# Performance work log

Hardware: AMD Instinct MI355X
Metric: run time of the kernel (lower is better)

## Reference

```python
import jax, jax.numpy as jnp
import numpy as np

B, BARS, BEATS, FRAC = 64, 16, 4, 8
IN_F = 10 * 47 * 2  # 940
LIN_OUT = 100
BEAT_H = 16
BAR_H = 32


def _p(key, shape, scale=0.05):
    return jax.random.normal(key, shape, dtype=jnp.float32) * scale


def setup_inputs() -> dict:
    key = jax.random.key(0)
    ks = jax.random.split(key, 16)
    return {
        "channels": jax.random.normal(ks[0], (B, BARS, BEATS, FRAC, 10, 2, 47), dtype=jnp.float32),
        "lin_w": _p(ks[1], (LIN_OUT, IN_F)),
        "lin_b": _p(ks[2], (LIN_OUT,)),
        # beats LSTM (unidirectional), PyTorch gate order i,f,g,o
        "b_wih": _p(ks[3], (4 * BEAT_H, LIN_OUT)),
        "b_whh": _p(ks[4], (4 * BEAT_H, BEAT_H)),
        "b_bih": _p(ks[5], (4 * BEAT_H,)),
        "b_bhh": _p(ks[6], (4 * BEAT_H,)),
        # bars LSTM, bidirectional: forward (f_) and reverse (r_) directions
        "f_wih": _p(ks[7], (4 * BAR_H, BEAT_H)),
        "f_whh": _p(ks[8], (4 * BAR_H, BAR_H)),
        "f_bih": _p(ks[9], (4 * BAR_H,)),
        "f_bhh": _p(ks[10], (4 * BAR_H,)),
        "r_wih": _p(ks[11], (4 * BAR_H, BEAT_H)),
        "r_whh": _p(ks[12], (4 * BAR_H, BAR_H)),
        "r_bih": _p(ks[13], (4 * BAR_H,)),
        "r_bhh": _p(ks[14], (4 * BAR_H,)),
    }


def lstm(x, wih, whh, bih, bhh):
    """PyTorch-semantics LSTM, batch_first. x: [N, T, F] -> h_seq [N, T, H]."""
    N = x.shape[0]
    H = whh.shape[1]
    # precompute input contribution for all timesteps
    xg = jnp.einsum('ntf,gf->ntg', x, wih) + (bih + bhh)  # [N, T, 4H]

    def step(carry, xt):
        h, c = carry
        gates = xt + h @ whh.T  # [N, 4H]
        i, f, g, o = jnp.split(gates, 4, axis=-1)
        c = jax.nn.sigmoid(f) * c + jax.nn.sigmoid(i) * jnp.tanh(g)
        h = jax.nn.sigmoid(o) * jnp.tanh(c)
        return (h, c), h

    h0 = jnp.zeros((N, H), x.dtype)
    _, hs = jax.lax.scan(step, (h0, h0), jnp.swapaxes(xg, 0, 1))  # [T, N, H]
    return jnp.swapaxes(hs, 0, 1)


def bilstm(x, f_wih, f_whh, f_bih, f_bhh, r_wih, r_whh, r_bih, r_bhh):
    fwd = lstm(x, f_wih, f_whh, f_bih, f_bhh)
    bwd = jnp.flip(lstm(jnp.flip(x, axis=1), r_wih, r_whh, r_bih, r_bhh), axis=1)
    return jnp.concatenate([fwd, bwd], axis=-1)


def reference(channels, lin_w, lin_b,
              b_wih, b_whh, b_bih, b_bhh,
              f_wih, f_whh, f_bih, f_bhh,
              r_wih, r_whh, r_bih, r_bhh):
    # channels: [B, bars, beats, frac, 10, 2, 47]
    x = jnp.swapaxes(channels, -1, -2)  # [..., 10, 47, 2]
    x = x.reshape(*x.shape[:4], IN_F)   # squash dims 4..6 -> 940
    x = jax.nn.relu(x @ lin_w.T + lin_b)  # [B, bars, beats, frac, 100]

    # Distributed depth=2: fold (B, bars, beats) into batch, seq over frac
    xb = x.reshape(B * BARS * BEATS, FRAC, LIN_OUT)
    beats = lstm(xb, b_wih, b_whh, b_bih, b_bhh)
    beats = beats.reshape(B, BARS, BEATS, FRAC, BEAT_H)

    # last fraction hidden state, then Distributed depth=1 over beats axis
    xl = beats[:, :, :, -1].reshape(B * BARS, BEATS, BEAT_H)
    bars = bilstm(xl, f_wih, f_whh, f_bih, f_bhh, r_wih, r_whh, r_bih, r_bhh)
    bars = bars.reshape(B, BARS, BEATS, 2 * BAR_H)
    return beats, bars
```

## Files before the change

### kernel.cpp

```cpp
#include <hip/hip_runtime.h>
#include <hip/hip_bf16.h>

typedef float f32x4 __attribute__((ext_vector_type(4)));
typedef short bf16x8 __attribute__((ext_vector_type(8)));

#define MFMA16(a, b, c) __builtin_amdgcn_mfma_f32_16x16x32_bf16(a, b, c, 0, 0, 0)

constexpr int K1  = 940;
constexpr int KP2 = 1024;
constexpr int NP  = 112;
constexpr int OSL = 136;
constexpr int BSR = 72;

__device__ __forceinline__ float sigf(float x) { return 1.f / (1.f + __expf(-x)); }
__device__ __forceinline__ float tanhfast(float x) { return 2.f / (1.f + __expf(-2.f * x)) - 1.f; }

__device__ __forceinline__ short f2b(float x) {
  __hip_bfloat16 b = __float2bfloat16(x);
  return *reinterpret_cast<short*>(&b);
}

__global__ void prep_kernel(const float* __restrict__ lin_w,
                            const float* __restrict__ b_wih,
                            __hip_bfloat16* __restrict__ w2,
                            __hip_bfloat16* __restrict__ bw2) {
  int idx = blockIdx.x * 256 + threadIdx.x;
  if (idx < NP * KP2) {
    int n = idx >> 10, k = idx & 1023;
    float v = 0.f;
    if (n < 100 && k < K1) {
      int c10 = k / 94, rem = k - c10 * 94;
      int c2 = rem / 47, c47 = rem - c2 * 47;
      int f = c10 * 94 + c47 * 2 + c2;
      v = lin_w[n * K1 + f];
    }
    w2[idx] = __float2bfloat16(v);
  } else {
    int i2 = idx - NP * KP2;
    if (i2 < 64 * 128) {
      int g = i2 >> 7, k = i2 & 127;
      bw2[i2] = __float2bfloat16((k < 100) ? b_wih[g * 100 + k] : 0.f);
    }
  }
}

__global__ __launch_bounds__(256, 2)
void fused_encoder(const float* __restrict__ ch,
                   const __hip_bfloat16* __restrict__ w2,
                   const float* __restrict__ lin_b,
                   const __hip_bfloat16* __restrict__ bw2,
                   const float* __restrict__ bih,
                   const float* __restrict__ bhh,
                   const float* __restrict__ whh,
                   float* __restrict__ beats) {
  __shared__ __align__(16) char smem[34048];
  __hip_bfloat16* Bs    = reinterpret_cast<__hip_bfloat16*>(smem);
  __hip_bfloat16* out_s = reinterpret_cast<__hip_bfloat16*>(smem);
  float*          xg_s  = reinterpret_cast<float*>(smem + 17408);

  const int tid = threadIdx.x;
  const int w = tid >> 6, lane = tid & 63;
  const int l16 = lane & 15, bq = lane >> 4;

  const int mbase = blockIdx.x * 64 + w * 16;
  const float* ar = ch + (long)(mbase + l16) * K1 + bq * 8;

  float lb[7];
#pragma unroll
  for (int nt = 0; nt < 7; ++nt) {
    int col = nt * 16 + l16;
    lb[nt] = (col < 100) ? lin_b[col] : 0.f;
  }

  auto mk = [&](float4 lo, float4 hi) -> bf16x8 {
    return bf16x8{f2b(lo.x), f2b(lo.y), f2b(lo.z), f2b(lo.w),
                  f2b(hi.x), f2b(hi.y), f2b(hi.z), f2b(hi.w)};
  };

  f32x4 acc[7] = {};
  float4 Ab[2][4];
  bf16x8 bst[4];

  const float4 f40{0.f, 0.f, 0.f, 0.f};
  auto ldA = [&](int c, float4* d) {
    const float* p = ar + c * 64;
    if (c < 14) {
      d[0] = *reinterpret_cast<const float4*>(p);
      d[1] = *reinterpret_cast<const float4*>(p + 4);
      d[2] = *reinterpret_cast<const float4*>(p + 32);
      d[3] = *reinterpret_cast<const float4*>(p + 36);
    } else {
      d[0] = *reinterpret_cast<const float4*>(p);
      d[1] = *reinterpret_cast<const float4*>(p + 4);
      d[2] = (bq <= 1) ? *reinterpret_cast<const float4*>(p + 32) : f40;
      d[3] = (bq == 0) ? *reinterpret_cast<const float4*>(p + 36) : f40;
    }
  };

  const int sn = tid >> 1, skh = (tid & 1) * 32;
  auto stageB_ld = [&](int c) {
    if (sn < NP) {
      const __hip_bfloat16* src = w2 + sn * KP2 + c * 64 + skh;
#pragma unroll
      for (int j = 0; j < 4; ++j)
        bst[j] = *reinterpret_cast<const bf16x8*>(src + j * 8);
    }
  };
  auto stageB_st = [&](int buf) {
    if (sn < NP) {
      __hip_bfloat16* dst = Bs + buf * (NP * BSR) + sn * BSR + skh;
#pragma unroll
      for (int j = 0; j < 4; ++j)
        *reinterpret_cast<bf16x8*>(dst + j * 8) = bst[j];
    }
  };

  stageB_ld(0);
  stageB_st(0);
  ldA(0, Ab[0]);
  __syncthreads();

  for (int c = 0; c < 15; ++c) {
    if (c < 14) {
      stageB_ld(c + 1);
      ldA(c + 1, Ab[(c + 1) & 1]);
    }
    const __hip_bfloat16* Bc = Bs + (c & 1) * (NP * BSR);
    float4* A = Ab[c & 1];
#pragma unroll
    for (int ks = 0; ks < 2; ++ks) {
      bf16x8 bf[7];
#pragma unroll
      for (int nt = 0; nt < 7; ++nt)
        bf[nt] = *reinterpret_cast<const bf16x8*>(
            &Bc[(nt * 16 + l16) * BSR + ks * 32 + bq * 8]);
      bf16x8 a = mk(A[2 * ks], A[2 * ks + 1]);
#pragma unroll
      for (int nt = 0; nt < 7; ++nt) acc[nt] = MFMA16(a, bf[nt], acc[nt]);
    }
    if (c < 14) stageB_st((c + 1) & 1);
    __syncthreads();
  }

#pragma unroll
  for (int nt = 0; nt < 7; ++nt) {
    const int col = nt * 16 + l16;
#pragma unroll
    for (int r = 0; r < 4; ++r) {
      float v = fmaxf(acc[nt][r] + lb[nt], 0.f);
      out_s[(w * 16 + bq * 4 + r) * OSL + col] = __float2bfloat16((col < 100) ? v : 0.f);
    }
  }
#pragma unroll
  for (int r = 0; r < 4; ++r)
    out_s[(w * 16 + bq * 4 + r) * OSL + 112 + l16] = __float2bfloat16(0.f);

  {
    bf16x8 av[4];
#pragma unroll
    for (int s = 0; s < 4; ++s)
      av[s] = *reinterpret_cast<const bf16x8*>(&out_s[(w * 16 + l16) * OSL + s * 32 + bq * 8]);
    f32x4 xacc[4] = {};
#pragma unroll
    for (int gt = 0; gt < 4; ++gt) {
#pragma unroll
      for (int s = 0; s < 4; ++s) {
        bf16x8 b = *reinterpret_cast<const bf16x8*>(&bw2[(gt * 16 + l16) * 128 + s * 32 + bq * 8]);
        xacc[gt] = MFMA16(av[s], b, xacc[gt]);
      }
    }
#pragma unroll
    for (int gt = 0; gt < 4; ++gt) {
      const int gate = gt * 16 + l16;
      const float bias = bih[gate] + bhh[gate];
#pragma unroll
      for (int r = 0; r < 4; ++r)
        xg_s[(w * 16 + bq * 4 + r) * 65 + gate] = xacc[gt][r] + bias;
    }
  }

  {
    const int cell = lane & 15;
    float wr[16];
#pragma unroll
    for (int u = 0; u < 16; ++u) wr[u] = whh[lane * 16 + u];
    float xv0[8], xv1[8];
#pragma unroll
    for (int t = 0; t < 8; ++t) {
      xv0[t] = xg_s[(w * 16 + t) * 65 + lane];
      xv1[t] = xg_s[(w * 16 + 8 + t) * 65 + lane];
    }
    float h0[16], h1[16];
#pragma unroll
    for (int u = 0; u < 16; ++u) { h0[u] = 0.f; h1[u] = 0.f; }
    float c0 = 0.f, c1 = 0.f;
    const long sg0 = (long)blockIdx.x * 8 + 2 * w;
    const long sg1 = sg0 + 1;
#pragma unroll
    for (int t = 0; t < 8; ++t) {
      float p0 = xv0[t], p1 = xv1[t];
#pragma unroll
      for (int u = 0; u < 16; ++u) { p0 += wr[u] * h0[u]; p1 += wr[u] * h1[u]; }
      const bool istanh = (lane >= 32 && lane < 48);
      float a0 = istanh ? tanhfast(p0) : sigf(p0);
      float a1 = istanh ? tanhfast(p1) : sigf(p1);
      float gi0 = __shfl(a0, cell),      gi1 = __shfl(a1, cell);
      float gf0 = __shfl(a0, cell + 16), gf1 = __shfl(a1, cell + 16);
      float gg0 = __shfl(a0, cell + 32), gg1 = __shfl(a1, cell + 32);
      float go0 = __shfl(a0, cell + 48), go1 = __shfl(a1, cell + 48);
      c0 = gf0 * c0 + gi0 * gg0;
      c1 = gf1 * c1 + gi1 * gg1;
      float hn0 = go0 * tanhfast(c0);
      float hn1 = go1 * tanhfast(c1);
#pragma unroll
      for (int u = 0; u < 16; ++u) { h0[u] = __shfl(hn0, u); h1[u] = __shfl(hn1, u); }
      if (lane < 16) {
        beats[sg0 * 128 + t * 16 + lane] = hn0;
        beats[sg1 * 128 + t * 16 + lane] = hn1;
      }
    }
  }
}

__global__ __launch_bounds__(256)
void bars_bilstm(const float* __restrict__ fwih, const float* __restrict__ fwhh,
                 const float* __restrict__ fbih, const float* __restrict__ fbhh,
                 const float* __restrict__ rwih, const float* __restrict__ rwhh,
                 const float* __restrict__ rbih, const float* __restrict__ rbhh,
                 const float* __restrict__ beats,
                 float* __restrict__ bars) {
  const int tid = threadIdx.x;
  const int dir = tid >> 7, g = tid & 127;
  const int n = blockIdx.x;
  const float* wih = dir ? rwih : fwih;
  const float* whh = dir ? rwhh : fwhh;
  const float bias = dir ? (rbih[g] + rbhh[g]) : (fbih[g] + fbhh[g]);
  float wi[16], wh[32];
#pragma unroll
  for (int u = 0; u < 16; ++u) wi[u] = wih[g * 16 + u];
#pragma unroll
  for (int u = 0; u < 32; ++u) wh[u] = whh[g * 32 + u];
  __shared__ float xbuf[2][16];
  __shared__ float hbuf[2][32];
  __shared__ float gact[2][128];
  float c = 0.f;
  if (g < 32) hbuf[dir][g] = 0.f;
  __syncthreads();
  for (int t = 0; t < 4; ++t) {
    const int tt = dir ? (3 - t) : t;
    if (g < 16) xbuf[dir][g] = beats[((n * 4 + tt) * 8 + 7) * 16 + g];
    __syncthreads();
    float pre = bias;
#pragma unroll
    for (int u = 0; u < 16; ++u) pre += wi[u] * xbuf[dir][u];
#pragma unroll
    for (int u = 0; u < 32; ++u) pre += wh[u] * hbuf[dir][u];
    gact[dir][g] = (g >= 64 && g < 96) ? tanhfast(pre) : sigf(pre);
    __syncthreads();
    if (g < 32) {
      c = gact[dir][32 + g] * c + gact[dir][g] * gact[dir][64 + g];
      float hn = gact[dir][96 + g] * tanhfast(c);
      hbuf[dir][g] = hn;
      bars[(n * 4 + tt) * 64 + dir * 32 + g] = hn;
    }
    __syncthreads();
  }
}

extern "C" void kernel_launch(void* const* d_in, const int* in_sizes, int n_in,
                              void* d_out, int out_size, void* d_ws, size_t ws_size,
                              hipStream_t stream) {
  const float* ch    = (const float*)d_in[0];
  const float* lin_w = (const float*)d_in[1];
  const float* lin_b = (const float*)d_in[2];
  const float* b_wih = (const float*)d_in[3];
  const float* b_whh = (const float*)d_in[4];
  const float* b_bih = (const float*)d_in[5];
  const float* b_bhh = (const float*)d_in[6];
  const float* f_wih = (const float*)d_in[7];
  const float* f_whh = (const float*)d_in[8];
  const float* f_bih = (const float*)d_in[9];
  const float* f_bhh = (const float*)d_in[10];
  const float* r_wih = (const float*)d_in[11];
  const float* r_whh = (const float*)d_in[12];
  const float* r_bih = (const float*)d_in[13];
  const float* r_bhh = (const float*)d_in[14];

  char* ws = (char*)d_ws;
  __hip_bfloat16* w2  = (__hip_bfloat16*)ws;
  __hip_bfloat16* bw2 = (__hip_bfloat16*)(ws + 229376);
  float*          out = (float*)d_out;

  prep_kernel<<<480, 256, 0, stream>>>(lin_w, b_wih, w2, bw2);
  fused_encoder<<<512, 256, 0, stream>>>(ch, w2, lin_b, bw2, b_bih, b_bhh,
                                         b_whh, out);
  bars_bilstm<<<1024, 256, 0, stream>>>(f_wih, f_whh, f_bih, f_bhh,
                                        r_wih, r_whh, r_bih, r_bhh,
                                        out, out + 524288);
}
```

Before: 230.4 us.

## Fuse bars BiLSTM into encoder kernel and double GEMM K-chunk size

Removes the separate bars_bilstm launch. Each encoder block now saves the last-fraction hidden states of its 8 sequences in shared memory, then runs the bidirectional bars LSTM for its 2 bar groups, so no round trip through global memory is needed. The GEMM main loop also moves from 64-wide to 128-wide K chunks, halving loop iterations and barriers. The cost is more registers for the staging buffers, a larger shared-memory footprint (about 69 KB) that may cut occupancy below the 2 blocks per CU the launch bounds ask for, and a serial BiLSTM tail inside each block.

```diff
diff --git a/kernel.cpp b/kernel.cpp
--- a/kernel.cpp
+++ b/kernel.cpp
@@ -10,7 +10,8 @@
 constexpr int KP2 = 1024;
 constexpr int NP  = 112;
 constexpr int OSL = 136;
-constexpr int BSR = 72;
+constexpr int BSR = 136;
+constexpr int BUFE = NP * BSR;
 
 __device__ __forceinline__ float sigf(float x) { return 1.f / (1.f + __expf(-x)); }
 __device__ __forceinline__ float tanhfast(float x) { return 2.f / (1.f + __expf(-2.f * x)) - 1.f; }
@@ -52,11 +53,19 @@
                    const float* __restrict__ bih,
                    const float* __restrict__ bhh,
                    const float* __restrict__ whh,
-                   float* __restrict__ beats) {
-  __shared__ __align__(16) char smem[34048];
+                   const float* __restrict__ fwih, const float* __restrict__ fwhh,
+                   const float* __restrict__ fbih, const float* __restrict__ fbhh,
+                   const float* __restrict__ rwih, const float* __restrict__ rwhh,
+                   const float* __restrict__ rbih, const float* __restrict__ rbhh,
+                   float* __restrict__ beats,
+                   float* __restrict__ bars) {
+  __shared__ __align__(16) char smem[2 * BUFE * 2];
   __hip_bfloat16* Bs    = reinterpret_cast<__hip_bfloat16*>(smem);
   __hip_bfloat16* out_s = reinterpret_cast<__hip_bfloat16*>(smem);
   float*          xg_s  = reinterpret_cast<float*>(smem + 17408);
+  float (*hlast)[16]    = reinterpret_cast<float(*)[16]>(smem + 34048);
+  float (*hb)[32]       = reinterpret_cast<float(*)[32]>(smem + 34560);
+  float (*gact)[128]    = reinterpret_cast<float(*)[128]>(smem + 34816);
 
   const int tid = threadIdx.x;
   const int w = tid >> 6, lane = tid & 63;
@@ -78,39 +87,41 @@
   };
 
   f32x4 acc[7] = {};
-  float4 Ab[2][4];
-  bf16x8 bst[4];
+  float4 Ab[2][8];
+  bf16x8 bst[8];
 
   const float4 f40{0.f, 0.f, 0.f, 0.f};
   auto ldA = [&](int c, float4* d) {
-    const float* p = ar + c * 64;
-    if (c < 14) {
-      d[0] = *reinterpret_cast<const float4*>(p);
-      d[1] = *reinterpret_cast<const float4*>(p + 4);
-      d[2] = *reinterpret_cast<const float4*>(p + 32);
-      d[3] = *reinterpret_cast<const float4*>(p + 36);
+    const float* p = ar + c * 128;
+    if (c < 7) {
+#pragma unroll
+      for (int ks = 0; ks < 4; ++ks) {
+        d[2 * ks]     = *reinterpret_cast<const float4*>(p + ks * 32);
+        d[2 * ks + 1] = *reinterpret_cast<const float4*>(p + ks * 32 + 4);
+      }
     } else {
       d[0] = *reinterpret_cast<const float4*>(p);
       d[1] = *reinterpret_cast<const float4*>(p + 4);
       d[2] = (bq <= 1) ? *reinterpret_cast<const float4*>(p + 32) : f40;
       d[3] = (bq == 0) ? *reinterpret_cast<const float4*>(p + 36) : f40;
+      d[4] = d[5] = d[6] = d[7] = f40;
     }
   };
 
-  const int sn = tid >> 1, skh = (tid & 1) * 32;
+  const int sn = tid >> 1, kh = (tid & 1) * 64;
   auto stageB_ld = [&](int c) {
     if (sn < NP) {
-      const __hip_bfloat16* src = w2 + sn * KP2 + c * 64 + skh;
-#pragma unroll
-      for (int j = 0; j < 4; ++j)
+      const __hip_bfloat16* src = w2 + sn * KP2 + c * 128 + kh;
+#pragma unroll
+      for (int j = 0; j < 8; ++j)
         bst[j] = *reinterpret_cast<const bf16x8*>(src + j * 8);
     }
   };
   auto stageB_st = [&](int buf) {
     if (sn < NP) {
-      __hip_bfloat16* dst = Bs + buf * (NP * BSR) + sn * BSR + skh;
-#pragma unroll
-      for (int j = 0; j < 4; ++j)
+      __hip_bfloat16* dst = Bs + buf * BUFE + sn * BSR + kh;
+#pragma unroll
+      for (int j = 0; j < 8; ++j)
         *reinterpret_cast<bf16x8*>(dst + j * 8) = bst[j];
     }
   };
@@ -120,15 +131,15 @@
   ldA(0, Ab[0]);
   __syncthreads();
 
-  for (int c = 0; c < 15; ++c) {
-    if (c < 14) {
+  for (int c = 0; c < 8; ++c) {
+    if (c < 7) {
       stageB_ld(c + 1);
       ldA(c + 1, Ab[(c + 1) & 1]);
     }
-    const __hip_bfloat16* Bc = Bs + (c & 1) * (NP * BSR);
+    const __hip_bfloat16* Bc = Bs + (c & 1) * BUFE;
     float4* A = Ab[c & 1];
 #pragma unroll
-    for (int ks = 0; ks < 2; ++ks) {
+    for (int ks = 0; ks < 4; ++ks) {
       bf16x8 bf[7];
 #pragma unroll
       for (int nt = 0; nt < 7; ++nt)
@@ -138,7 +149,7 @@
 #pragma unroll
       for (int nt = 0; nt < 7; ++nt) acc[nt] = MFMA16(a, bf[nt], acc[nt]);
     }
-    if (c < 14) stageB_st((c + 1) & 1);
+    if (c < 7) stageB_st((c + 1) & 1);
     __syncthreads();
   }
 
@@ -217,53 +228,48 @@
       if (lane < 16) {
         beats[sg0 * 128 + t * 16 + lane] = hn0;
         beats[sg1 * 128 + t * 16 + lane] = hn1;
+        if (t == 7) {
+          hlast[2 * w][lane]     = hn0;
+          hlast[2 * w + 1][lane] = hn1;
+        }
       }
     }
   }
-}
-
-__global__ __launch_bounds__(256)
-void bars_bilstm(const float* __restrict__ fwih, const float* __restrict__ fwhh,
-                 const float* __restrict__ fbih, const float* __restrict__ fbhh,
-                 const float* __restrict__ rwih, const float* __restrict__ rwhh,
-                 const float* __restrict__ rbih, const float* __restrict__ rbhh,
-                 const float* __restrict__ beats,
-                 float* __restrict__ bars) {
-  const int tid = threadIdx.x;
-  const int dir = tid >> 7, g = tid & 127;
-  const int n = blockIdx.x;
-  const float* wih = dir ? rwih : fwih;
-  const float* whh = dir ? rwhh : fwhh;
-  const float bias = dir ? (rbih[g] + rbhh[g]) : (fbih[g] + fbhh[g]);
-  float wi[16], wh[32];
-#pragma unroll
-  for (int u = 0; u < 16; ++u) wi[u] = wih[g * 16 + u];
-#pragma unroll
-  for (int u = 0; u < 32; ++u) wh[u] = whh[g * 32 + u];
-  __shared__ float xbuf[2][16];
-  __shared__ float hbuf[2][32];
-  __shared__ float gact[2][128];
-  float c = 0.f;
-  if (g < 32) hbuf[dir][g] = 0.f;
   __syncthreads();
-  for (int t = 0; t < 4; ++t) {
-    const int tt = dir ? (3 - t) : t;
-    if (g < 16) xbuf[dir][g] = beats[((n * 4 + tt) * 8 + 7) * 16 + g];
-    __syncthreads();
-    float pre = bias;
-#pragma unroll
-    for (int u = 0; u < 16; ++u) pre += wi[u] * xbuf[dir][u];
-#pragma unroll
-    for (int u = 0; u < 32; ++u) pre += wh[u] * hbuf[dir][u];
-    gact[dir][g] = (g >= 64 && g < 96) ? tanhfast(pre) : sigf(pre);
-    __syncthreads();
-    if (g < 32) {
-      c = gact[dir][32 + g] * c + gact[dir][g] * gact[dir][64 + g];
-      float hn = gact[dir][96 + g] * tanhfast(c);
-      hbuf[dir][g] = hn;
-      bars[(n * 4 + tt) * 64 + dir * 32 + g] = hn;
-    }
-    __syncthreads();
+
+  {
+    const int dir = tid >> 7, g = tid & 127;
+    const float* wihp = dir ? rwih : fwih;
+    const float* whhp = dir ? rwhh : fwhh;
+    const float bias = dir ? (rbih[g] + rbhh[g]) : (fbih[g] + fbhh[g]);
+    float wi[16], wh[32];
+#pragma unroll
+    for (int u = 0; u < 16; ++u) wi[u] = wihp[g * 16 + u];
+#pragma unroll
+    for (int u = 0; u < 32; ++u) wh[u] = whhp[g * 32 + u];
+    for (int b2 = 0; b2 < 2; ++b2) {
+      const int n = blockIdx.x * 2 + b2;
+      float c = 0.f;
+      if (g < 32) hb[dir][g] = 0.f;
+      __syncthreads();
+      for (int t = 0; t < 4; ++t) {
+        const int tt = dir ? (3 - t) : t;
+        float pre = bias;
+#pragma unroll
+        for (int u = 0; u < 16; ++u) pre += wi[u] * hlast[b2 * 4 + tt][u];
+#pragma unroll
+        for (int u = 0; u < 32; ++u) pre += wh[u] * hb[dir][u];
+        gact[dir][g] = (g >= 64 && g < 96) ? tanhfast(pre) : sigf(pre);
+        __syncthreads();
+        if (g < 32) {
+          c = gact[dir][32 + g] * c + gact[dir][g] * gact[dir][64 + g];
+          float hn = gact[dir][96 + g] * tanhfast(c);
+          hb[dir][g] = hn;
+          bars[(n * 4 + tt) * 64 + dir * 32 + g] = hn;
+        }
+        __syncthreads();
+      }
+    }
   }
 }
 
@@ -293,8 +299,8 @@
 
   prep_kernel<<<480, 256, 0, stream>>>(lin_w, b_wih, w2, bw2);
   fused_encoder<<<512, 256, 0, stream>>>(ch, w2, lin_b, bw2, b_bih, b_bhh,
-                                         b_whh, out);
-  bars_bilstm<<<1024, 256, 0, stream>>>(f_wih, f_whh, f_bih, f_bhh,
-                                        r_wih, r_whh, r_bih, r_bhh,
-                                        out, out + 524288);
+                                         b_whh,
+                                         f_wih, f_whh, f_bih, f_bhh,
+                                         r_wih, r_whh, r_bih, r_bhh,
+                                         out, out + 524288);
 }
```

Result: no change. 227.9 us (-1.1%).
